# Optimization experiments

Measured on AMD Instinct MI355X. Metric: run time of the kernel, lower is better.

Reference implementation:

```python
import jax, jax.numpy as jnp
import numpy as np

B, E, C, K, H, OUT = 8192, 16, 256, 2, 64, 387

def setup_inputs() -> dict:
    ks = jax.random.split(jax.random.key(0), 6)
    x = jax.random.normal(ks[0], (B, E, C), dtype=jnp.float32)
    adj = jax.random.normal(ks[1], (E, E), dtype=jnp.float32) * (6.0 / (E + E)) ** 0.5  # xavier-ish
    adj_bias = jax.random.normal(ks[2], (1,), dtype=jnp.float32) * 0.1
    cheb_w = jax.random.normal(ks[3], (K * C, H), dtype=jnp.float32) * (6.0 / (K * C + H)) ** 0.5
    brelu_bias = jnp.zeros((1, 1, H), dtype=jnp.float32)
    fc_w = jax.random.normal(ks[4], (OUT, H), dtype=jnp.float32) * (1.0 / H) ** 0.5
    fc_b = jax.random.normal(ks[5], (OUT,), dtype=jnp.float32) * (1.0 / H) ** 0.5
    return {"x": x, "adj": adj, "adj_bias": adj_bias, "cheb_w": cheb_w,
            "brelu_bias": brelu_bias, "fc_w": fc_w, "fc_b": fc_b}

def reference(x, adj, adj_bias, cheb_w, brelu_bias, fc_w, fc_b):
    # adaptive adjacency + biased ReLU (Eq. 4 prelude)
    w = jax.nn.relu(adj + adj_bias)  # (E,E)
    # normalized Laplacian: I - D^{-1/2} W D^{-1/2}
    d_re = 1.0 / jnp.sqrt(jnp.sum(w, axis=1) + 1e-5)  # (E,)
    lap = jnp.eye(E, dtype=x.dtype) - d_re[:, None] * w * d_re[None, :]  # (E,E)
    # Chebyshev polynomial, k=2: T0 = ones, T1 = lap @ x
    t0 = jnp.ones_like(x)                       # (B,E,C)
    t1 = jnp.einsum('ij,bjc->bic', lap, x)      # (B,E,C)
    # torch: stack on dim=1 -> permute(0,2,3,1) -> flatten(2)  == interleave along last axis
    cp = jnp.stack([t0, t1], axis=-1).reshape(B, E, K * C)  # (B,E,K*C)
    h = jnp.einsum('bek,kh->beh', cp, cheb_w)   # (B,E,H)
    # dropout is identity at eval
    h = jax.nn.relu(brelu_bias + h)
    out = jnp.einsum('beh,oh->beo', h, fc_w) + fc_b  # (B,E,OUT)
    return out
```

## Files before the change

### kernel.cpp

```cpp
#include <hip/hip_runtime.h>
#include <stdint.h>


typedef __attribute__((ext_vector_type(4))) float f32x4;
typedef __attribute__((ext_vector_type(8))) short s16x8;
typedef __attribute__((ext_vector_type(4))) short s16x4;

#define WS_CH_B    0
#define WS_LAP_B   256
#define WS_LAPA_B  1280
#define WS_FCB_B   1792
#define WS_W1T_B   4096
#define WS_FCW_B   36864
#define FCW_ROWS   400

static __device__ __forceinline__ short f2bf(float f) {
    union { float f; uint32_t u; } v; v.f = f;
    uint32_t r = (v.u + 0x7fffu + ((v.u >> 16) & 1u)) >> 16;
    return (short)r;
}

__global__ void prep_kernel(const float* __restrict__ adj,
                            const float* __restrict__ adj_bias,
                            const float* __restrict__ cheb_w,
                            const float* __restrict__ brelu_bias,
                            const float* __restrict__ fc_w,
                            const float* __restrict__ fc_b,
                            char* __restrict__ ws) {
    float* chf  = (float*)(ws + WS_CH_B);
    float* lapf = (float*)(ws + WS_LAP_B);
    short* lapA = (short*)(ws + WS_LAPA_B);
    float* fcbp = (float*)(ws + WS_FCB_B);
    short* w1t  = (short*)(ws + WS_W1T_B);
    short* fcw  = (short*)(ws + WS_FCW_B);
    int t = threadIdx.x;

    if (blockIdx.x == 0) {
        __shared__ float sw[16][17];
        __shared__ float sdre[16];
        __shared__ float slap[16][16];
        __shared__ float csum[4][64];
        float ab = adj_bias[0];
        {
            int i = t >> 4, j = t & 15;
            sw[i][j] = fmaxf(adj[t] + ab, 0.f);
        }
        {
            int hh = t & 63, part = t >> 6;
            float s = 0.f;
            #pragma unroll 8
            for (int i = 0; i < 64; ++i) s += cheb_w[(2 * (part * 64 + i)) * 64 + hh];
            csum[part][hh] = s;
        }
        __syncthreads();
        if (t < 16) {
            float s = 0.f;
            #pragma unroll
            for (int j = 0; j < 16; ++j) s += sw[t][j];
            sdre[t] = 1.0f / sqrtf(s + 1e-5f);
        }
        __syncthreads();
        {
            int i = t >> 4, j = t & 15;
            float l = (i == j ? 1.f : 0.f) - sdre[i] * sw[i][j] * sdre[j];
            slap[i][j] = l;
            lapf[t] = l;
        }
        __syncthreads();
        if (t < 64) {
            int m = t & 15, qq = t >> 4;
            #pragma unroll
            for (int i = 0; i < 4; ++i)
                lapA[t * 4 + i] = f2bf(slap[m][qq * 4 + i]);
            chf[t] = csum[0][t] + csum[1][t] + csum[2][t] + csum[3][t] + brelu_bias[t];
        }
        for (int o = t; o < 400; o += 256) fcbp[o] = (o < 387) ? fc_b[o] : 0.f;
    }
    int gt = blockIdx.x * blockDim.x + t;
    int nthr = gridDim.x * blockDim.x;
    for (int idx = gt; idx < 64 * 256; idx += nthr) {
        int hh = idx >> 8, c = idx & 255;
        w1t[idx] = f2bf(cheb_w[(2 * c + 1) * 64 + hh]);
    }
    for (int idx = gt; idx < FCW_ROWS * 64; idx += nthr) {
        fcw[idx] = (idx < 387 * 64) ? f2bf(fc_w[idx]) : (short)0;
    }
}

__global__ __launch_bounds__(256, 4) void fused_kernel(
        const float* __restrict__ x,
        const char* __restrict__ ws,
        float* __restrict__ out) {
    const float* chf  = (const float*)(ws + WS_CH_B);
    const short* lapA = (const short*)(ws + WS_LAPA_B);
    const float* fcbp = (const float*)(ws + WS_FCB_B);
    const short* w1t  = (const short*)(ws + WS_W1T_B);
    const short* fcw  = (const short*)(ws + WS_FCW_B);

    __shared__ __align__(16) short hs[4][16][72];

    const int lane = threadIdx.x & 63;
    const int wave = threadIdx.x >> 6;
    const int n = lane & 15;
    const int q = lane >> 4;
    const long b = (long)blockIdx.x * 4 + wave;

    const float* xb = x + b * 4096;

    const float* xrow = xb + n * 256 + q * 8;
    f32x4 xr[16];
    #pragma unroll
    for (int kb = 0; kb < 8; ++kb) {
        xr[2 * kb]     = *(const f32x4*)(xrow + kb * 32);
        xr[2 * kb + 1] = *(const f32x4*)(xrow + kb * 32 + 4);
    }
    s16x8 af[8];
    #pragma unroll
    for (int kb = 0; kb < 8; ++kb) {
        f32x4 xa = xr[2 * kb], xc = xr[2 * kb + 1];
        af[kb][0] = f2bf(xa[0]); af[kb][1] = f2bf(xa[1]);
        af[kb][2] = f2bf(xa[2]); af[kb][3] = f2bf(xa[3]);
        af[kb][4] = f2bf(xc[0]); af[kb][5] = f2bf(xc[1]);
        af[kb][6] = f2bf(xc[2]); af[kb][7] = f2bf(xc[3]);
    }
    f32x4 g[4];
    #pragma unroll
    for (int nt = 0; nt < 4; ++nt) g[nt] = (f32x4){0.f, 0.f, 0.f, 0.f};
    #pragma unroll
    for (int kb = 0; kb < 8; ++kb) {
        const int k0 = kb * 32 + q * 8;
        #pragma unroll
        for (int nt = 0; nt < 4; ++nt) {
            s16x8 bf = *(const s16x8*)(w1t + (nt * 16 + n) * 256 + k0);
            g[nt] = __builtin_amdgcn_mfma_f32_16x16x32_bf16(af[kb], bf, g[nt], 0, 0, 0);
        }
    }

    f32x4 h[4];
#if defined(__has_builtin) && __has_builtin(__builtin_amdgcn_mfma_f32_16x16x16bf16_1k)
    {
        s16x4 la = *(const s16x4*)(lapA + lane * 4);
        const f32x4 z4 = (f32x4){0.f, 0.f, 0.f, 0.f};
        #pragma unroll
        for (int nt = 0; nt < 4; ++nt) {
            s16x4 gb;
            gb[0] = f2bf(g[nt][0]); gb[1] = f2bf(g[nt][1]);
            gb[2] = f2bf(g[nt][2]); gb[3] = f2bf(g[nt][3]);
            h[nt] = __builtin_amdgcn_mfma_f32_16x16x16bf16_1k(la, gb, z4, 0, 0, 0);
        }
    }
#else
    {
        __shared__ float gs[4][16][68];
        const float* lapf = (const float*)(ws + WS_LAP_B);
        #pragma unroll
        for (int r = 0; r < 4; ++r) {
            gs[wave][q * 4 + r][0 * 16 + n] = g[0][r];
            gs[wave][q * 4 + r][1 * 16 + n] = g[1][r];
            gs[wave][q * 4 + r][2 * 16 + n] = g[2][r];
            gs[wave][q * 4 + r][3 * 16 + n] = g[3][r];
        }
        __syncthreads();
        #pragma unroll
        for (int nt = 0; nt < 4; ++nt) h[nt] = (f32x4){0.f, 0.f, 0.f, 0.f};
        #pragma unroll
        for (int e = 0; e < 16; ++e) {
            float l0 = lapf[(q * 4 + 0) * 16 + e];
            float l1 = lapf[(q * 4 + 1) * 16 + e];
            float l2 = lapf[(q * 4 + 2) * 16 + e];
            float l3 = lapf[(q * 4 + 3) * 16 + e];
            #pragma unroll
            for (int nt = 0; nt < 4; ++nt) {
                float gv = gs[wave][e][nt * 16 + n];
                h[nt][0] += l0 * gv; h[nt][1] += l1 * gv;
                h[nt][2] += l2 * gv; h[nt][3] += l3 * gv;
            }
        }
    }
#endif

    #pragma unroll
    for (int nt = 0; nt < 4; ++nt) {
        float cv = chf[nt * 16 + n];
        #pragma unroll
        for (int r = 0; r < 4; ++r) {
            float v = fmaxf(h[nt][r] + cv, 0.f);
            hs[wave][q * 4 + r][nt * 16 + n] = f2bf(v);
        }
    }
    __syncthreads();

    s16x8 ha0 = *(const s16x8*)(&hs[wave][n][q * 8]);
    s16x8 ha1 = *(const s16x8*)(&hs[wave][n][32 + q * 8]);
    float* outb = out + (b * 16 + q * 4) * 387;
    #pragma unroll
    for (int tt = 0; tt < 25; ++tt) {
        const int o0 = tt * 16;
        s16x8 fb0 = *(const s16x8*)(fcw + (o0 + n) * 64 + q * 8);
        s16x8 fb1 = *(const s16x8*)(fcw + (o0 + n) * 64 + 32 + q * 8);
        const int o = o0 + n;
        float bias = fcbp[o];
        f32x4 acc = (f32x4){bias, bias, bias, bias};
        acc = __builtin_amdgcn_mfma_f32_16x16x32_bf16(ha0, fb0, acc, 0, 0, 0);
        acc = __builtin_amdgcn_mfma_f32_16x16x32_bf16(ha1, fb1, acc, 0, 0, 0);
        if (o < 387) {
            outb[0 * 387 + o] = acc[0];
            outb[1 * 387 + o] = acc[1];
            outb[2 * 387 + o] = acc[2];
            outb[3 * 387 + o] = acc[3];
        }
    }
}

extern "C" void kernel_launch(void* const* d_in, const int* in_sizes, int n_in,
                              void* d_out, int out_size, void* d_ws, size_t ws_size,
                              hipStream_t stream) {
    const float* x          = (const float*)d_in[0];
    const float* adj        = (const float*)d_in[1];
    const float* adj_bias   = (const float*)d_in[2];
    const float* cheb_w     = (const float*)d_in[3];
    const float* brelu_bias = (const float*)d_in[4];
    const float* fc_w       = (const float*)d_in[5];
    const float* fc_b       = (const float*)d_in[6];
    float* outp = (float*)d_out;
    char* ws = (char*)d_ws;

    prep_kernel<<<64, 256, 0, stream>>>(adj, adj_bias, cheb_w, brelu_bias, fc_w, fc_b, ws);
    fused_kernel<<<2048, 256, 0, stream>>>(x, ws, outp);
}
```

Baseline: 389.1 us.

## Pre-swizzle weights into MFMA fragment layout and double-buffer fragment loads

The prep kernel now stores cheb_w and fc_w as per-lane MFMA fragments, so each lane in the fused kernel reads 16 contiguous bytes at a uniform stride instead of doing strided row gathers. Weight fragments for the first GEMM and the output GEMM are prefetched into double-buffered registers one step ahead of the MFMAs, overlapping global loads with matrix math. The __syncthreads before the output stage becomes a per-wave LDS waitcnt, since each wave only reads its own hs slice, and the occupancy hint is removed from launch_bounds. The prefetch buffers raise register pressure and may reduce occupancy. The waitcnt-only handoff also depends on the wave's LDS writes being visible to its own later reads.

```diff
diff --git a/kernel.cpp b/kernel.cpp
--- a/kernel.cpp
+++ b/kernel.cpp
@@ -10,9 +10,8 @@
 #define WS_LAP_B   256
 #define WS_LAPA_B  1280
 #define WS_FCB_B   1792
-#define WS_W1T_B   4096
-#define WS_FCW_B   36864
-#define FCW_ROWS   400
+#define WS_W1T2_B  4096
+#define WS_FCW2_B  36864
 
 static __device__ __forceinline__ short f2bf(float f) {
     union { float f; uint32_t u; } v; v.f = f;
@@ -31,8 +30,8 @@
     float* lapf = (float*)(ws + WS_LAP_B);
     short* lapA = (short*)(ws + WS_LAPA_B);
     float* fcbp = (float*)(ws + WS_FCB_B);
-    short* w1t  = (short*)(ws + WS_W1T_B);
-    short* fcw  = (short*)(ws + WS_FCW_B);
+    short* w1t2 = (short*)(ws + WS_W1T2_B);
+    short* fcw2 = (short*)(ws + WS_FCW2_B);
     int t = threadIdx.x;
 
     if (blockIdx.x == 0) {
@@ -78,24 +77,33 @@
     }
     int gt = blockIdx.x * blockDim.x + t;
     int nthr = gridDim.x * blockDim.x;
-    for (int idx = gt; idx < 64 * 256; idx += nthr) {
-        int hh = idx >> 8, c = idx & 255;
-        w1t[idx] = f2bf(cheb_w[(2 * c + 1) * 64 + hh]);
-    }
-    for (int idx = gt; idx < FCW_ROWS * 64; idx += nthr) {
-        fcw[idx] = (idx < 387 * 64) ? f2bf(fc_w[idx]) : (short)0;
-    }
-}
-
-__global__ __launch_bounds__(256, 4) void fused_kernel(
+    for (int idx = gt; idx < 32 * 512; idx += nthr) {
+        int frag = idx >> 9, r = idx & 511;
+        int lane = r >> 3, j = r & 7;
+        int kb = frag >> 2, nt = frag & 3;
+        int k = kb * 32 + (lane >> 4) * 8 + j;
+        int col = nt * 16 + (lane & 15);
+        w1t2[idx] = f2bf(cheb_w[(2 * k + 1) * 64 + col]);
+    }
+    for (int idx = gt; idx < 50 * 512; idx += nthr) {
+        int frag = idx >> 9, r = idx & 511;
+        int lane = r >> 3, j = r & 7;
+        int tt = frag >> 1, f = frag & 1;
+        int o = tt * 16 + (lane & 15);
+        int k = f * 32 + (lane >> 4) * 8 + j;
+        fcw2[idx] = (o < 387) ? f2bf(fc_w[o * 64 + k]) : (short)0;
+    }
+}
+
+__global__ __launch_bounds__(256) void fused_kernel(
         const float* __restrict__ x,
         const char* __restrict__ ws,
         float* __restrict__ out) {
     const float* chf  = (const float*)(ws + WS_CH_B);
     const short* lapA = (const short*)(ws + WS_LAPA_B);
     const float* fcbp = (const float*)(ws + WS_FCB_B);
-    const short* w1t  = (const short*)(ws + WS_W1T_B);
-    const short* fcw  = (const short*)(ws + WS_FCW_B);
+    const short* w1t2 = (const short*)(ws + WS_W1T2_B);
+    const short* fcw2 = (const short*)(ws + WS_FCW2_B);
 
     __shared__ __align__(16) short hs[4][16][72];
 
@@ -105,9 +113,7 @@
     const int q = lane >> 4;
     const long b = (long)blockIdx.x * 4 + wave;
 
-    const float* xb = x + b * 4096;
-
-    const float* xrow = xb + n * 256 + q * 8;
+    const float* xrow = x + b * 4096 + n * 256 + q * 8;
     f32x4 xr[16];
     #pragma unroll
     for (int kb = 0; kb < 8; ++kb) {
@@ -123,17 +129,25 @@
         af[kb][4] = f2bf(xc[0]); af[kb][5] = f2bf(xc[1]);
         af[kb][6] = f2bf(xc[2]); af[kb][7] = f2bf(xc[3]);
     }
+    const short* w1 = w1t2 + lane * 8;
+    s16x8 bfr[2][4];
+    #pragma unroll
+    for (int nt = 0; nt < 4; ++nt)
+        bfr[0][nt] = *(const s16x8*)(w1 + nt * 512);
     f32x4 g[4];
     #pragma unroll
     for (int nt = 0; nt < 4; ++nt) g[nt] = (f32x4){0.f, 0.f, 0.f, 0.f};
     #pragma unroll
     for (int kb = 0; kb < 8; ++kb) {
-        const int k0 = kb * 32 + q * 8;
-        #pragma unroll
-        for (int nt = 0; nt < 4; ++nt) {
-            s16x8 bf = *(const s16x8*)(w1t + (nt * 16 + n) * 256 + k0);
-            g[nt] = __builtin_amdgcn_mfma_f32_16x16x32_bf16(af[kb], bf, g[nt], 0, 0, 0);
-        }
+        const int cur = kb & 1;
+        if (kb < 7) {
+            #pragma unroll
+            for (int nt = 0; nt < 4; ++nt)
+                bfr[cur ^ 1][nt] = *(const s16x8*)(w1 + ((kb + 1) * 4 + nt) * 512);
+        }
+        #pragma unroll
+        for (int nt = 0; nt < 4; ++nt)
+            g[nt] = __builtin_amdgcn_mfma_f32_16x16x32_bf16(af[kb], bfr[cur][nt], g[nt], 0, 0, 0);
     }
 
     f32x4 h[4];
@@ -188,26 +202,42 @@
             hs[wave][q * 4 + r][nt * 16 + n] = f2bf(v);
         }
     }
-    __syncthreads();
-
+    __builtin_amdgcn_s_waitcnt(0xC07F);
+
+    const short* fw = fcw2 + lane * 8;
+    s16x8 fb[2][10];
+    #pragma unroll
+    for (int t = 0; t < 5; ++t) {
+        fb[0][2 * t]     = *(const s16x8*)(fw + (t * 2 + 0) * 512);
+        fb[0][2 * t + 1] = *(const s16x8*)(fw + (t * 2 + 1) * 512);
+    }
     s16x8 ha0 = *(const s16x8*)(&hs[wave][n][q * 8]);
     s16x8 ha1 = *(const s16x8*)(&hs[wave][n][32 + q * 8]);
     float* outb = out + (b * 16 + q * 4) * 387;
     #pragma unroll
-    for (int tt = 0; tt < 25; ++tt) {
-        const int o0 = tt * 16;
-        s16x8 fb0 = *(const s16x8*)(fcw + (o0 + n) * 64 + q * 8);
-        s16x8 fb1 = *(const s16x8*)(fcw + (o0 + n) * 64 + 32 + q * 8);
-        const int o = o0 + n;
-        float bias = fcbp[o];
-        f32x4 acc = (f32x4){bias, bias, bias, bias};
-        acc = __builtin_amdgcn_mfma_f32_16x16x32_bf16(ha0, fb0, acc, 0, 0, 0);
-        acc = __builtin_amdgcn_mfma_f32_16x16x32_bf16(ha1, fb1, acc, 0, 0, 0);
-        if (o < 387) {
-            outb[0 * 387 + o] = acc[0];
-            outb[1 * 387 + o] = acc[1];
-            outb[2 * 387 + o] = acc[2];
-            outb[3 * 387 + o] = acc[3];
+    for (int c = 0; c < 5; ++c) {
+        if (c < 4) {
+            #pragma unroll
+            for (int t = 0; t < 5; ++t) {
+                int tt = (c + 1) * 5 + t;
+                fb[(c + 1) & 1][2 * t]     = *(const s16x8*)(fw + (tt * 2 + 0) * 512);
+                fb[(c + 1) & 1][2 * t + 1] = *(const s16x8*)(fw + (tt * 2 + 1) * 512);
+            }
+        }
+        #pragma unroll
+        for (int t = 0; t < 5; ++t) {
+            const int tt = c * 5 + t;
+            const int o = tt * 16 + n;
+            float bias = fcbp[o];
+            f32x4 acc = (f32x4){bias, bias, bias, bias};
+            acc = __builtin_amdgcn_mfma_f32_16x16x32_bf16(ha0, fb[c & 1][2 * t], acc, 0, 0, 0);
+            acc = __builtin_amdgcn_mfma_f32_16x16x32_bf16(ha1, fb[c & 1][2 * t + 1], acc, 0, 0, 0);
+            if (o < 387) {
+                outb[0 * 387 + o] = acc[0];
+                outb[1 * 387 + o] = acc[1];
+                outb[2 * 387 + o] = acc[2];
+                outb[3 * 387 + o] = acc[3];
+            }
         }
     }
 }
```

Measured after the change: 345.6 us. 11.2% less time.
